# Kernel optimization log

Hardware: AMD Instinct MI355X
Metric: run time of the kernel (lower is better)

Reference implementation:

```python
import jax, jax.numpy as jnp
import numpy as np

N_FRAMES = 4
HEADS = 8
SEQ = 576
DIM = 640


def setup_inputs() -> dict:
    key = jax.random.key(0)
    ks = jax.random.split(key, 6)
    x = jax.random.normal(ks[0], (3 * N_FRAMES, SEQ, DIM), dtype=jnp.float32)
    s = 1.0 / np.sqrt(DIM)
    Wq = jax.random.normal(ks[1], (DIM, DIM), dtype=jnp.float32) * s
    Wk = jax.random.normal(ks[2], (DIM, DIM), dtype=jnp.float32) * s
    Wv = jax.random.normal(ks[3], (DIM, DIM), dtype=jnp.float32) * s
    Wo = jax.random.normal(ks[4], (DIM, DIM), dtype=jnp.float32) * s
    bo = jnp.zeros((DIM,), dtype=jnp.float32)
    return {"x": x, "Wq": Wq, "Wk": Wk, "Wv": Wv, "Wo": Wo, "bo": bo}


def reference(x, Wq, Wk, Wv, Wo, bo):
    # x: [3F, S, D] -- stacked [source | uncond | cond] frame batches
    B, S, D = x.shape
    n = B // 3                       # n_frames
    h = HEADS
    hd = D // h
    scale = 1.0 / jnp.sqrt(jnp.asarray(hd, x.dtype))

    # torch nn.Linear: y = x @ W.T
    q = jnp.einsum('bsd,ed->bse', x, Wq)
    k = jnp.einsum('bsd,ed->bse', x, Wk)
    v = jnp.einsum('bsd,ed->bse', x, Wv)

    def heads_fd(t):  # [F,S,D] -> [F,h,S,hd]
        return t.reshape(t.shape[0], S, h, hd).transpose(0, 2, 1, 3)

    def heads_flat(t):  # [F,S,D] -> [h, F*S, hd]  (shared across all query frames)
        return t.reshape(t.shape[0] * S, h, hd).transpose(1, 0, 2)

    # ---- source: per-frame self-attention ----
    qs, ks_, vs = heads_fd(q[:n]), heads_fd(k[:n]), heads_fd(v[:n])
    sim_s = jnp.einsum('fhqd,fhkd->fhqk', qs, ks_) * scale
    out_s = jnp.einsum('fhqk,fhkd->fhqd', jax.nn.softmax(sim_s, axis=-1), vs)

    # ---- uncond / cond: each frame attends to concatenated KV of all frames ----
    def cross_frame(q_chunk, k_chunk, v_chunk):
        qf = heads_fd(q_chunk)          # [F,h,S,hd]
        kf = heads_flat(k_chunk)        # [h,F*S,hd]
        vf = heads_flat(v_chunk)        # [h,F*S,hd]
        sim = jnp.einsum('fhqd,hkd->fhqk', qf, kf) * scale   # [F,h,S,F*S]
        return jnp.einsum('fhqk,hkd->fhqd', jax.nn.softmax(sim, axis=-1), vf)

    out_u = cross_frame(q[n:2 * n], k[n:2 * n], v[n:2 * n])
    out_c = cross_frame(q[2 * n:], k[2 * n:], v[2 * n:])

    out = jnp.concatenate([out_s, out_u, out_c], axis=0)      # [3F,h,S,hd]
    out = out.transpose(0, 2, 1, 3).reshape(B, S, D)          # merge heads
    return jnp.einsum('bsd,ed->bse', out, Wo) + bo
```

## Files before the change

### kernel.cpp

```cpp
#include <hip/hip_runtime.h>
#include <hip/hip_bf16.h>

#define SEQ    576
#define DIM    640
#define HEADS  8
#define HD     80
#define NF     4
#define NB     12
#define M_TOT  (NB * SEQ)
#define SCALE  0.11180339887498949f
#define LOG2E  1.4426950408889634f

typedef __attribute__((ext_vector_type(8))) short          bf16x8;
typedef __attribute__((ext_vector_type(4))) float          f32x4;
typedef __attribute__((ext_vector_type(8))) unsigned short u16x8;
typedef __attribute__((ext_vector_type(4))) unsigned short u16x4;

__device__ __forceinline__ unsigned short f2bf(float x) {
    unsigned u = __float_as_uint(x);
    u += 0x7fffu + ((u >> 16) & 1u);
    return (unsigned short)(u >> 16);
}
__device__ __forceinline__ float bf2f(unsigned short h) {
    return __uint_as_float((unsigned)h << 16);
}
__device__ __forceinline__ f32x4 mfma16(bf16x8 a, bf16x8 b, f32x4 c) {
    return __builtin_amdgcn_mfma_f32_16x16x32_bf16(a, b, c, 0, 0, 0);
}
__device__ __forceinline__ float fexp2(float x) {
    return __builtin_amdgcn_exp2f(x);
}
__device__ __forceinline__ void dma16(const void* g, void* s) {
    __builtin_amdgcn_global_load_lds(
        (const __attribute__((address_space(1))) void*)g,
        (__attribute__((address_space(3))) void*)s, 16, 0, 0);
}

__global__ __launch_bounds__(256) void split_kernel(
    const float* __restrict__ X,  const float* __restrict__ Wq,
    const float* __restrict__ Wk, const float* __restrict__ Wv,
    const float* __restrict__ Wo,
    unsigned short* __restrict__ Xh,  unsigned short* __restrict__ Wqh,
    unsigned short* __restrict__ Wkh, unsigned short* __restrict__ Wvh,
    unsigned short* __restrict__ Woh)
{
    const int z = blockIdx.y;
    const float* src; unsigned short* dh; int n; float s = 1.0f;
    switch (z) {
        case 0:  src = X;  dh = Xh;  n = M_TOT * DIM; break;
        case 1:  src = Wq; dh = Wqh; n = DIM * DIM; s = SCALE * LOG2E; break;
        case 2:  src = Wk; dh = Wkh; n = DIM * DIM; break;
        case 3:  src = Wv; dh = Wvh; n = DIM * DIM; break;
        default: src = Wo; dh = Woh; n = DIM * DIM; break;
    }
    const int base = blockIdx.x * 4096 + threadIdx.x * 16;
    if (base >= n) return;
#pragma unroll
    for (int half = 0; half < 2; ++half) {
        const int b = base + half * 8;
        float4 a4 = *(const float4*)(src + b);
        float4 b4 = *(const float4*)(src + b + 4);
        float vv[8] = {a4.x, a4.y, a4.z, a4.w, b4.x, b4.y, b4.z, b4.w};
        union { unsigned short u[8]; u16x8 v; } ph;
#pragma unroll
        for (int j = 0; j < 8; ++j) ph.u[j] = f2bf(vv[j] * s);
        *(u16x8*)(dh + b) = ph.v;
    }
}

__global__ __launch_bounds__(256) void qkv_mfma_kernel(
    const unsigned short* __restrict__ Xh,
    const unsigned short* __restrict__ Wqh, const unsigned short* __restrict__ Wkh,
    const unsigned short* __restrict__ Wvh,
    unsigned short* __restrict__ Qh,
    unsigned short* __restrict__ Kb, unsigned short* __restrict__ VtG)
{
    __shared__ unsigned short smem[2][10240];

    const int flat = blockIdx.x + 27 * (blockIdx.y + 10 * blockIdx.z);
    const int xcd  = flat & 7;
    const int slot = flat >> 3;
    const int l    = (xcd < 2 ? xcd * 102 : 204 + (xcd - 2) * 101) + slot;
    const int m_idx = l / 30;
    const int rem   = l - m_idx * 30;
    const int z     = rem / 10;
    const int n_idx = rem - z * 10;

    const unsigned short* WH = (z == 0) ? Wqh : ((z == 1) ? Wkh : Wvh);
    const int m0 = m_idx * 256;
    const int n0 = n_idx * 64;

    const int t    = threadIdx.x;
    const int w    = t >> 6;
    const int lane = t & 63;
    const int quad = lane >> 4;
    const int ln   = lane & 15;

    f32x4 acc[4][4];
#pragma unroll
    for (int mi = 0; mi < 4; ++mi)
#pragma unroll
        for (int nt = 0; nt < 4; ++nt)
#pragma unroll
            for (int e = 0; e < 4; ++e) acc[mi][nt][e] = 0.f;

    const int lr = lane >> 2;
    const int lc = (lane & 3) * 8;

    auto stage = [&](int buf, int k0) {
        unsigned short* As = smem[buf];
        unsigned short* Bs = smem[buf] + 8192;
        const unsigned short* gp = Xh + (size_t)(m0 + w * 64 + lr) * DIM + k0 + lc;
#pragma unroll
        for (int i = 0; i < 4; ++i)
            dma16(gp + (size_t)i * 16 * DIM, &As[(w * 64 + i * 16) * 32]);
        const size_t gb = (size_t)(n0 + w * 16 + lr) * DIM + k0 + lc;
        dma16(WH + gb, &Bs[w * 16 * 32]);
    };

    stage(0, 0);
    __syncthreads();

    for (int k0 = 0; k0 < DIM; k0 += 32) {
        const int kb = (k0 >> 5) & 1;
        if (k0 + 32 < DIM) stage(kb ^ 1, k0 + 32);

        const unsigned short* As = smem[kb];
        const unsigned short* Bs = smem[kb] + 8192;
        bf16x8 af[4];
#pragma unroll
        for (int mi = 0; mi < 4; ++mi)
            af[mi] = *(const bf16x8*)&As[(w * 64 + mi * 16 + ln) * 32 + quad * 8];
#pragma unroll
        for (int nt = 0; nt < 4; ++nt) {
            bf16x8 bh = *(const bf16x8*)&Bs[(nt * 16 + ln) * 32 + quad * 8];
#pragma unroll
            for (int mi = 0; mi < 4; ++mi)
                acc[mi][nt] = mfma16(af[mi], bh, acc[mi][nt]);
        }
        __syncthreads();
    }

    if (z == 0) {
#pragma unroll
        for (int mi = 0; mi < 4; ++mi)
#pragma unroll
            for (int r = 0; r < 4; ++r) {
                const size_t row = m0 + w * 64 + mi * 16 + quad * 4 + r;
#pragma unroll
                for (int nt = 0; nt < 4; ++nt)
                    Qh[row * DIM + n0 + nt * 16 + ln] = f2bf(acc[mi][nt][r]);
            }
    } else if (z == 1) {
#pragma unroll
        for (int mi = 0; mi < 4; ++mi)
#pragma unroll
            for (int r = 0; r < 4; ++r) {
                const size_t row = m0 + w * 64 + mi * 16 + quad * 4 + r;
#pragma unroll
                for (int nt = 0; nt < 4; ++nt)
                    Kb[row * DIM + n0 + nt * 16 + ln] = f2bf(acc[mi][nt][r]);
            }
    } else {
        unsigned short* Vts = smem[0];
#pragma unroll 1
        for (int half = 0; half < 2; ++half) {
            __syncthreads();
            if ((w >> 1) == half) {
                const int wl = w & 1;
#pragma unroll
                for (int mi = 0; mi < 4; ++mi)
#pragma unroll
                    for (int nt = 0; nt < 4; ++nt)
#pragma unroll
                        for (int r = 0; r < 4; ++r)
                            Vts[(nt * 16 + ln) * 136 + wl * 64 + mi * 16 + quad * 4 + r] =
                                f2bf(acc[mi][nt][r]);
            }
            __syncthreads();
            const int nn = t & 63;
            const int c0 = (t >> 6) * 32;
#pragma unroll
            for (int i = 0; i < 4; ++i)
                *(u16x8*)(VtG + (size_t)(n0 + nn) * M_TOT + m0 + half * 128 + c0 + i * 8) =
                    *(const u16x8*)&Vts[nn * 136 + c0 + i * 8];
        }
    }
}

__global__ __launch_bounds__(256, 2) void attn_mfma_kernel(
    const unsigned short* __restrict__ Qh,
    const unsigned short* __restrict__ Kb, const unsigned short* __restrict__ Vt,
    unsigned short* __restrict__ Oh,
    unsigned short* __restrict__ Pn, float2* __restrict__ ml)
{
    const int flat = blockIdx.x + 3 * (blockIdx.y + 8 * blockIdx.z);
    const int h    = flat & 7;
    const int slot = flat >> 3;
    const int z    = slot / 3;
    const int qt   = slot - z * 3;

    int f, kbase, nkt, idx = -1;
    if (z < 24) {
        idx = z;
        const int fi = z / 3;
        const int part = z - fi * 3;
        f = 4 + fi;
        kbase = (fi < 4 ? 4 : 8) * SEQ + part * 12 * 64;
        nkt = 12;
    } else {
        f = z - 24;
        kbase = f * SEQ;
        nkt = 9;
    }

    const int t    = threadIdx.x;
    const int w    = t >> 6;
    const int lane = t & 63;
    const int quad = lane >> 4;
    const int ln   = lane & 15;

    __shared__ unsigned short KhS[2][12 * 64 * 8];
    __shared__ unsigned short VtS[2][80 * 64];
    __shared__ unsigned short Pb[4 * 48 * 72];

    bf16x8 qf[3][3];
#pragma unroll
    for (int mi = 0; mi < 3; ++mi) {
        const int qrow = f * SEQ + qt * 192 + w * 48 + mi * 16 + ln;
        const unsigned short* qp = Qh + (size_t)qrow * DIM + h * HD;
#pragma unroll
        for (int kc = 0; kc < 3; ++kc) {
            const int dbase = kc * 32 + quad * 8;
            if (dbase < HD) {
                qf[mi][kc] = *(const bf16x8*)(qp + dbase);
            } else {
                union { unsigned short u[8]; bf16x8 v; } zz;
#pragma unroll
                for (int j = 0; j < 8; ++j) zz.u[j] = 0;
                qf[mi][kc] = zz.v;
            }
        }
    }

    auto stage_k = [&](int buf, int kvt) {
        const unsigned short* kg = Kb + (size_t)(kbase + kvt * 64) * DIM + h * HD;
#pragma unroll
        for (int rnd = 0; rnd < 3; ++rnd) {
            const int g = rnd * 4 + w;
            dma16(kg + (size_t)lane * DIM + g * 8, &KhS[buf][g * 512]);
        }
    };
    u16x8 vreg[3];
    auto load_v = [&](int kvt) {
#pragma unroll
        for (int i = 0; i < 3; ++i) {
            const int u = t + i * 256;
            if (u < 640) {
                const int d = u >> 3, c8 = u & 7;
                vreg[i] = *(const u16x8*)(Vt + (size_t)(h * HD + d) * M_TOT +
                                          kbase + kvt * 64 + c8 * 8);
            }
        }
    };
    auto write_v = [&](int buf) {
#pragma unroll
        for (int i = 0; i < 3; ++i) {
            const int u = t + i * 256;
            if (u < 640) {
                const int d = u >> 3, c8 = u & 7;
                const int c8s = (c8 + 3 * d) & 7;
                *(u16x8*)&VtS[buf][d * 64 + c8s * 8] = vreg[i];
            }
        }
    };

    float m_[3], l_[3];
#pragma unroll
    for (int mi = 0; mi < 3; ++mi) { m_[mi] = -INFINITY; l_[mi] = 0.f; }

    f32x4 oacc[3][5];
#pragma unroll
    for (int mi = 0; mi < 3; ++mi)
#pragma unroll
        for (int nt = 0; nt < 5; ++nt)
#pragma unroll
            for (int e = 0; e < 4; ++e) oacc[mi][nt][e] = 0.f;

    unsigned short* PbW = &Pb[w * 48 * 72];

    stage_k(0, 0);
    load_v(0);
    write_v(0);
    __syncthreads();

    for (int kt = 0; kt < nkt; ++kt) {
        const int cur = kt & 1;
        const bool pf = (kt + 1 < nkt);

        if (pf) {
            load_v(kt + 1);
            stage_k(cur ^ 1, kt + 1);
        }

        f32x4 sacc[3][4];
#pragma unroll
        for (int mi = 0; mi < 3; ++mi)
#pragma unroll
            for (int nt = 0; nt < 4; ++nt)
#pragma unroll
                for (int e = 0; e < 4; ++e) sacc[mi][nt][e] = 0.f;
        __builtin_amdgcn_s_setprio(1);
#pragma unroll
        for (int nt = 0; nt < 4; ++nt)
#pragma unroll
            for (int kc = 0; kc < 3; ++kc) {
                bf16x8 kf = *(const bf16x8*)&KhS[cur][((kc * 4 + quad) * 64 +
                                                      nt * 16 + ln) * 8];
#pragma unroll
                for (int mi = 0; mi < 3; ++mi)
                    sacc[mi][nt] = mfma16(kf, qf[mi][kc], sacc[mi][nt]);
            }
        __builtin_amdgcn_s_setprio(0);

        float mxl[3];
#pragma unroll
        for (int mi = 0; mi < 3; ++mi) {
            float t0[4];
#pragma unroll
            for (int nt = 0; nt < 4; ++nt)
                t0[nt] = fmaxf(fmaxf(sacc[mi][nt][0], sacc[mi][nt][1]),
                               fmaxf(sacc[mi][nt][2], sacc[mi][nt][3]));
            mxl[mi] = fmaxf(fmaxf(t0[0], t0[1]), fmaxf(t0[2], t0[3]));
        }
        const bool need = (mxl[0] > m_[0] + 8.0f) || (mxl[1] > m_[1] + 8.0f) ||
                          (mxl[2] > m_[2] + 8.0f);
        if (__any(need)) {
#pragma unroll
            for (int mi = 0; mi < 3; ++mi) {
                float mx = fmaxf(mxl[mi], __shfl_xor(mxl[mi], 16));
                mx = fmaxf(mx, __shfl_xor(mx, 32));
                const float mnew = fmaxf(m_[mi], mx);
                const float aq = fexp2(m_[mi] - mnew);
                m_[mi] = mnew;
                l_[mi] *= aq;
#pragma unroll
                for (int r = 0; r < 4; ++r) {
                    const float ar = __shfl(aq, quad * 4 + r, 64);
#pragma unroll
                    for (int nt = 0; nt < 5; ++nt) oacc[mi][nt][r] *= ar;
                }
            }
        }
#pragma unroll
        for (int mi = 0; mi < 3; ++mi) {
            float s = 0.f;
#pragma unroll
            for (int nt = 0; nt < 4; ++nt) {
                const float p0 = fexp2(sacc[mi][nt][0] - m_[mi]);
                const float p1 = fexp2(sacc[mi][nt][1] - m_[mi]);
                const float p2 = fexp2(sacc[mi][nt][2] - m_[mi]);
                const float p3 = fexp2(sacc[mi][nt][3] - m_[mi]);
                s += (p0 + p1) + (p2 + p3);
                union { unsigned u32[2]; u16x4 v; } pk;
                pk.u32[0] = __builtin_amdgcn_perm(__float_as_uint(p1),
                                                  __float_as_uint(p0), 0x07060302u);
                pk.u32[1] = __builtin_amdgcn_perm(__float_as_uint(p3),
                                                  __float_as_uint(p2), 0x07060302u);
                *(u16x4*)&PbW[(mi * 16 + ln) * 72 + nt * 16 + quad * 4] = pk.v;
            }
            l_[mi] += s;
        }

        __threadfence_block();

        __builtin_amdgcn_s_setprio(1);
#pragma unroll
        for (int kc = 0; kc < 2; ++kc) {
            bf16x8 pf_[3];
#pragma unroll
            for (int mi = 0; mi < 3; ++mi)
                pf_[mi] = *(const bf16x8*)&PbW[(mi * 16 + ln) * 72 + kc * 32 + quad * 8];
#pragma unroll
            for (int nt = 0; nt < 5; ++nt) {
                const int vrow = nt * 16 + ln;
                const int c8r  = ((kc * 4 + quad) + 3 * vrow) & 7;
                bf16x8 vf = *(const bf16x8*)&VtS[cur][vrow * 64 + c8r * 8];
#pragma unroll
                for (int mi = 0; mi < 3; ++mi)
                    oacc[mi][nt] = mfma16(pf_[mi], vf, oacc[mi][nt]);
            }
        }
        __builtin_amdgcn_s_setprio(0);

        if (pf) write_v(cur ^ 1);
        __syncthreads();
    }

#pragma unroll
    for (int mi = 0; mi < 3; ++mi) {
        l_[mi] += __shfl_xor(l_[mi], 16);
        l_[mi] += __shfl_xor(l_[mi], 32);
    }
#pragma unroll
    for (int mi = 0; mi < 3; ++mi)
#pragma unroll
        for (int r = 0; r < 4; ++r) {
            const float lr_ = __shfl(l_[mi], quad * 4 + r, 64);
            const float inv = 1.f / lr_;
            const int rr = qt * 192 + w * 48 + mi * 16 + quad * 4 + r;
            if (idx < 0) {
                const size_t orow = (size_t)f * SEQ + rr;
#pragma unroll
                for (int nt = 0; nt < 5; ++nt)
                    Oh[orow * DIM + h * HD + nt * 16 + ln] = f2bf(oacc[mi][nt][r] * inv);
            } else {
#pragma unroll
                for (int nt = 0; nt < 5; ++nt)
                    Pn[((size_t)idx * SEQ + rr) * DIM + h * HD + nt * 16 + ln] =
                        f2bf(oacc[mi][nt][r] * inv);
            }
        }
    if (idx >= 0 && lane < 16) {
#pragma unroll
        for (int mi = 0; mi < 3; ++mi) {
            const int rr = qt * 192 + w * 48 + mi * 16 + lane;
            ml[((size_t)idx * 8 + h) * SEQ + rr] = make_float2(m_[mi], l_[mi]);
        }
    }
}

__global__ __launch_bounds__(320) void merge_kernel(
    const unsigned short* __restrict__ Pn, const float2* __restrict__ ml,
    unsigned short* __restrict__ Oh)
{
    const int row = blockIdx.x;
    const int fi  = blockIdx.y;
    const int t   = threadIdx.x;
    const int i0  = fi * 3, i1 = i0 + 1, i2 = i0 + 2;
#pragma unroll
    for (int rep = 0; rep < 2; ++rep) {
        const int col = t + rep * 320;
        const int h = col / 80;
        const float2 a = ml[((size_t)i0 * 8 + h) * SEQ + row];
        const float2 b = ml[((size_t)i1 * 8 + h) * SEQ + row];
        const float2 c = ml[((size_t)i2 * 8 + h) * SEQ + row];
        const float M  = fmaxf(fmaxf(a.x, b.x), c.x);
        const float w0 = fexp2(a.x - M) * a.y;
        const float w1 = fexp2(b.x - M) * b.y;
        const float w2 = fexp2(c.x - M) * c.y;
        const float inv = 1.f / (w0 + w1 + w2);
        const float p0 = bf2f(Pn[((size_t)i0 * SEQ + row) * DIM + col]);
        const float p1 = bf2f(Pn[((size_t)i1 * SEQ + row) * DIM + col]);
        const float p2 = bf2f(Pn[((size_t)i2 * SEQ + row) * DIM + col]);
        Oh[((size_t)(4 + fi) * SEQ + row) * DIM + col] =
            f2bf((w0 * p0 + w1 * p1 + w2 * p2) * inv);
    }
}

__global__ __launch_bounds__(256) void oproj_mfma_kernel(
    const unsigned short* __restrict__ Oh,
    const unsigned short* __restrict__ Woh,
    const float* __restrict__ bo, float* __restrict__ out)
{
    __shared__ unsigned short smem[2][10240];

    const int flat = blockIdx.x + 27 * blockIdx.y;
    const int xcd  = flat & 7;
    const int slot = flat >> 3;
    const int l    = (xcd < 6 ? xcd * 34 : 204 + (xcd - 6) * 33) + slot;
    const int m_idx = l / 10;
    const int n_idx = l - m_idx * 10;
    const int m0 = m_idx * 256;
    const int n0 = n_idx * 64;

    const int t    = threadIdx.x;
    const int w    = t >> 6;
    const int lane = t & 63;
    const int quad = lane >> 4;
    const int ln   = lane & 15;

    f32x4 acc[4][4];
#pragma unroll
    for (int mi = 0; mi < 4; ++mi)
#pragma unroll
        for (int nt = 0; nt < 4; ++nt)
#pragma unroll
            for (int e = 0; e < 4; ++e) acc[mi][nt][e] = 0.f;

    const int lr = lane >> 2;
    const int lc = (lane & 3) * 8;

    auto stage = [&](int buf, int k0) {
        unsigned short* As = smem[buf];
        unsigned short* Bs = smem[buf] + 8192;
        const unsigned short* gp = Oh + (size_t)(m0 + w * 64 + lr) * DIM + k0 + lc;
#pragma unroll
        for (int i = 0; i < 4; ++i)
            dma16(gp + (size_t)i * 16 * DIM, &As[(w * 64 + i * 16) * 32]);
        const size_t gb = (size_t)(n0 + w * 16 + lr) * DIM + k0 + lc;
        dma16(Woh + gb, &Bs[w * 16 * 32]);
    };

    stage(0, 0);
    __syncthreads();

    for (int k0 = 0; k0 < DIM; k0 += 32) {
        const int kb = (k0 >> 5) & 1;
        if (k0 + 32 < DIM) stage(kb ^ 1, k0 + 32);

        const unsigned short* As = smem[kb];
        const unsigned short* Bs = smem[kb] + 8192;
        bf16x8 af[4];
#pragma unroll
        for (int mi = 0; mi < 4; ++mi)
            af[mi] = *(const bf16x8*)&As[(w * 64 + mi * 16 + ln) * 32 + quad * 8];
#pragma unroll
        for (int nt = 0; nt < 4; ++nt) {
            bf16x8 bh = *(const bf16x8*)&Bs[(nt * 16 + ln) * 32 + quad * 8];
#pragma unroll
            for (int mi = 0; mi < 4; ++mi)
                acc[mi][nt] = mfma16(af[mi], bh, acc[mi][nt]);
        }
        __syncthreads();
    }

#pragma unroll
    for (int mi = 0; mi < 4; ++mi)
#pragma unroll
        for (int r = 0; r < 4; ++r) {
            const size_t row = m0 + w * 64 + mi * 16 + quad * 4 + r;
#pragma unroll
            for (int nt = 0; nt < 4; ++nt) {
                const int col = n0 + nt * 16 + ln;
                out[row * DIM + col] = acc[mi][nt][r] + bo[col];
            }
        }
}

extern "C" void kernel_launch(void* const* d_in, const int* in_sizes, int n_in,
                              void* d_out, int out_size, void* d_ws, size_t ws_size,
                              hipStream_t stream)
{
    const float* x  = (const float*)d_in[0];
    const float* Wq = (const float*)d_in[1];
    const float* Wk = (const float*)d_in[2];
    const float* Wv = (const float*)d_in[3];
    const float* Wo = (const float*)d_in[4];
    const float* bo = (const float*)d_in[5];
    float* out = (float*)d_out;

    const size_t NX = (size_t)M_TOT * DIM;
    const size_t NW = (size_t)DIM * DIM;
    unsigned short* p = (unsigned short*)d_ws;
    unsigned short* Wqh = p;  p += NW;
    unsigned short* Wkh = p;  p += NW;
    unsigned short* Wvh = p;  p += NW;
    unsigned short* Woh = p;  p += NW;
    unsigned short* Xh  = p;  p += NX;
    unsigned short* Qhb = p;  p += NX;
    unsigned short* Kbb = p;  p += NX;
    unsigned short* Vtb = p;  p += NX;
    unsigned short* Ohb = Xh;

    unsigned short* Pn = (unsigned short*)d_out;
    float2* ml = (float2*)Wqh;

    dim3 g0((unsigned)((NX + 4095) / 4096), 5);
    split_kernel<<<g0, 256, 0, stream>>>(x, Wq, Wk, Wv, Wo,
        Xh, Wqh, Wkh, Wvh, Woh);

    dim3 g1(M_TOT / 256, DIM / 64, 3);
    qkv_mfma_kernel<<<g1, 256, 0, stream>>>(Xh, Wqh, Wkh, Wvh, Qhb, Kbb, Vtb);

    dim3 g2(3, HEADS, 28);
    attn_mfma_kernel<<<g2, 256, 0, stream>>>(Qhb, Kbb, Vtb, Ohb, Pn, ml);

    dim3 g3(SEQ, 8);
    merge_kernel<<<g3, 320, 0, stream>>>(Pn, ml, Ohb);

    dim3 g4(M_TOT / 256, DIM / 64);
    oproj_mfma_kernel<<<g4, 256, 0, stream>>>(Ohb, Woh, bo, out);
}
```

Baseline: 199.6 us.

## Shrink attention LDS footprint to fit three blocks per CU

Single-buffers the V tile and halves the per-wave P staging buffer so the P matrix is written and consumed in two 32-column halves. Launch bounds move to three blocks per CU to raise occupancy. The change also removes the s_setprio hints, folds the zero init of the score accumulators into the first MFMA, uses three-input max reductions, and replaces the thread fence with an explicit LDS waitcnt. The cost is an extra __syncthreads per KV tile, since V can no longer be double buffered, and tighter register limits that could cause spills.

```diff
diff --git a/kernel.cpp b/kernel.cpp
--- a/kernel.cpp
+++ b/kernel.cpp
@@ -29,6 +29,9 @@
 }
 __device__ __forceinline__ float fexp2(float x) {
     return __builtin_amdgcn_exp2f(x);
+}
+__device__ __forceinline__ float max3f(float a, float b, float c) {
+    return fmaxf(fmaxf(a, b), c);
 }
 __device__ __forceinline__ void dma16(const void* g, void* s) {
     __builtin_amdgcn_global_load_lds(
@@ -188,7 +191,7 @@
     }
 }
 
-__global__ __launch_bounds__(256, 2) void attn_mfma_kernel(
+__global__ __launch_bounds__(256, 3) void attn_mfma_kernel(
     const unsigned short* __restrict__ Qh,
     const unsigned short* __restrict__ Kb, const unsigned short* __restrict__ Vt,
     unsigned short* __restrict__ Oh,
@@ -206,7 +209,7 @@
         const int fi = z / 3;
         const int part = z - fi * 3;
         f = 4 + fi;
-        kbase = (fi < 4 ? 4 : 8) * SEQ + part * 12 * 64;
+        kbase = (fi < 4 ? 4 : 8) * SEQ + part * 768;
         nkt = 12;
     } else {
         f = z - 24;
@@ -221,8 +224,8 @@
     const int ln   = lane & 15;
 
     __shared__ unsigned short KhS[2][12 * 64 * 8];
-    __shared__ unsigned short VtS[2][80 * 64];
-    __shared__ unsigned short Pb[4 * 48 * 72];
+    __shared__ unsigned short VtS[80 * 64];
+    __shared__ unsigned short Pb[4 * 48 * 36];
 
     bf16x8 qf[3][3];
 #pragma unroll
@@ -263,14 +266,14 @@
             }
         }
     };
-    auto write_v = [&](int buf) {
+    auto write_v = [&]() {
 #pragma unroll
         for (int i = 0; i < 3; ++i) {
             const int u = t + i * 256;
             if (u < 640) {
                 const int d = u >> 3, c8 = u & 7;
                 const int c8s = (c8 + 3 * d) & 7;
-                *(u16x8*)&VtS[buf][d * 64 + c8s * 8] = vreg[i];
+                *(u16x8*)&VtS[d * 64 + c8s * 8] = vreg[i];
             }
         }
     };
@@ -287,11 +290,11 @@
 #pragma unroll
             for (int e = 0; e < 4; ++e) oacc[mi][nt][e] = 0.f;
 
-    unsigned short* PbW = &Pb[w * 48 * 72];
+    unsigned short* PbW = &Pb[w * 48 * 36];
 
     stage_k(0, 0);
     load_v(0);
-    write_v(0);
+    write_v();
     __syncthreads();
 
     for (int kt = 0; kt < nkt; ++kt) {
@@ -303,14 +306,8 @@
             stage_k(cur ^ 1, kt + 1);
         }
 
+        const f32x4 fz = {0.f, 0.f, 0.f, 0.f};
         f32x4 sacc[3][4];
-#pragma unroll
-        for (int mi = 0; mi < 3; ++mi)
-#pragma unroll
-            for (int nt = 0; nt < 4; ++nt)
-#pragma unroll
-                for (int e = 0; e < 4; ++e) sacc[mi][nt][e] = 0.f;
-        __builtin_amdgcn_s_setprio(1);
 #pragma unroll
         for (int nt = 0; nt < 4; ++nt)
 #pragma unroll
@@ -319,19 +316,21 @@
                                                       nt * 16 + ln) * 8];
 #pragma unroll
                 for (int mi = 0; mi < 3; ++mi)
-                    sacc[mi][nt] = mfma16(kf, qf[mi][kc], sacc[mi][nt]);
-            }
-        __builtin_amdgcn_s_setprio(0);
+                    sacc[mi][nt] = (kc == 0)
+                        ? mfma16(kf, qf[mi][0], fz)
+                        : mfma16(kf, qf[mi][kc], sacc[mi][nt]);
+            }
 
         float mxl[3];
 #pragma unroll
         for (int mi = 0; mi < 3; ++mi) {
-            float t0[4];
-#pragma unroll
-            for (int nt = 0; nt < 4; ++nt)
-                t0[nt] = fmaxf(fmaxf(sacc[mi][nt][0], sacc[mi][nt][1]),
-                               fmaxf(sacc[mi][nt][2], sacc[mi][nt][3]));
-            mxl[mi] = fmaxf(fmaxf(t0[0], t0[1]), fmaxf(t0[2], t0[3]));
+            const f32x4* S = sacc[mi];
+            const float a = max3f(S[0][0], S[0][1], S[0][2]);
+            const float b = max3f(S[0][3], S[1][0], S[1][1]);
+            const float c = max3f(S[1][2], S[1][3], S[2][0]);
+            const float d = max3f(S[2][1], S[2][2], S[2][3]);
+            const float e = max3f(S[3][0], S[3][1], S[3][2]);
+            mxl[mi] = fmaxf(max3f(a, b, c), max3f(d, e, S[3][3]));
         }
         const bool need = (mxl[0] > m_[0] + 8.0f) || (mxl[1] > m_[1] + 8.0f) ||
                           (mxl[2] > m_[2] + 8.0f);
@@ -352,6 +351,7 @@
                 }
             }
         }
+        unsigned pk[3][4][2];
 #pragma unroll
         for (int mi = 0; mi < 3; ++mi) {
             float s = 0.f;
@@ -362,38 +362,45 @@
                 const float p2 = fexp2(sacc[mi][nt][2] - m_[mi]);
                 const float p3 = fexp2(sacc[mi][nt][3] - m_[mi]);
                 s += (p0 + p1) + (p2 + p3);
-                union { unsigned u32[2]; u16x4 v; } pk;
-                pk.u32[0] = __builtin_amdgcn_perm(__float_as_uint(p1),
-                                                  __float_as_uint(p0), 0x07060302u);
-                pk.u32[1] = __builtin_amdgcn_perm(__float_as_uint(p3),
-                                                  __float_as_uint(p2), 0x07060302u);
-                *(u16x4*)&PbW[(mi * 16 + ln) * 72 + nt * 16 + quad * 4] = pk.v;
+                pk[mi][nt][0] = __builtin_amdgcn_perm(__float_as_uint(p1),
+                                                      __float_as_uint(p0), 0x07060302u);
+                pk[mi][nt][1] = __builtin_amdgcn_perm(__float_as_uint(p3),
+                                                      __float_as_uint(p2), 0x07060302u);
             }
             l_[mi] += s;
         }
 
-        __threadfence_block();
-
-        __builtin_amdgcn_s_setprio(1);
 #pragma unroll
         for (int kc = 0; kc < 2; ++kc) {
+#pragma unroll
+            for (int mi = 0; mi < 3; ++mi)
+#pragma unroll
+                for (int n2 = 0; n2 < 2; ++n2) {
+                    union { unsigned u32[2]; u16x4 v; } pq;
+                    pq.u32[0] = pk[mi][kc * 2 + n2][0];
+                    pq.u32[1] = pk[mi][kc * 2 + n2][1];
+                    *(u16x4*)&PbW[(mi * 16 + ln) * 36 + n2 * 16 + quad * 4] = pq.v;
+                }
+            __builtin_amdgcn_s_waitcnt(0xC07F);
+            __builtin_amdgcn_sched_barrier(0);
+
             bf16x8 pf_[3];
 #pragma unroll
             for (int mi = 0; mi < 3; ++mi)
-                pf_[mi] = *(const bf16x8*)&PbW[(mi * 16 + ln) * 72 + kc * 32 + quad * 8];
+                pf_[mi] = *(const bf16x8*)&PbW[(mi * 16 + ln) * 36 + quad * 8];
 #pragma unroll
             for (int nt = 0; nt < 5; ++nt) {
                 const int vrow = nt * 16 + ln;
                 const int c8r  = ((kc * 4 + quad) + 3 * vrow) & 7;
-                bf16x8 vf = *(const bf16x8*)&VtS[cur][vrow * 64 + c8r * 8];
+                bf16x8 vf = *(const bf16x8*)&VtS[vrow * 64 + c8r * 8];
 #pragma unroll
                 for (int mi = 0; mi < 3; ++mi)
                     oacc[mi][nt] = mfma16(pf_[mi], vf, oacc[mi][nt]);
             }
         }
-        __builtin_amdgcn_s_setprio(0);
-
-        if (pf) write_v(cur ^ 1);
+
+        __syncthreads();
+        if (pf) write_v();
         __syncthreads();
     }
 
```

Result: slower. 265.8 us (+33.2%).
